# Kernel tuning notes

Measured on AMD Instinct MI355X. Metric: run time of the kernel, lower is better.

The kernel has to match this reference:

```python
import jax, jax.numpy as jnp
import numpy as np

DIMS = [3, 64, 64, 64, 3]  # [input_dim] + hidden dims + [input_dim]
TOTAL_W = sum(DIMS[l] * DIMS[l + 1] + 4 * DIMS[l + 1] for l in range(len(DIMS) - 1))  # 9356


def setup_inputs() -> dict:
    key = jax.random.key(0)
    k1, k2, k3 = jax.random.split(key, 3)
    B, N = 64, 8192
    context = jax.random.normal(k1, (B, N), dtype=jnp.float32)
    y = jax.random.normal(k2, (B, N, DIMS[0]), dtype=jnp.float32)
    tnw = jax.random.normal(k3, (B, TOTAL_W), dtype=jnp.float32) * 0.1
    return {"context": context, "y": y, "target_networks_weights": tnw}


def reference(context, y, target_networks_weights):
    B = target_networks_weights.shape[0]
    dx = y  # [B, N, dims[0]]
    i = 0
    n_layers = len(DIMS) - 1
    for l in range(n_layers):
        dl, dl1 = DIMS[l], DIMS[l + 1]
        W = target_networks_weights[:, i:i + dl * dl1].reshape(B, dl, dl1)
        i += dl * dl1
        bias = target_networks_weights[:, i:i + dl1]          # [B, dl1]
        i += dl1
        w_scale = target_networks_weights[:, i:i + dl1]        # [B, dl1]
        i += dl1
        b_scale = target_networks_weights[:, i:i + dl1]        # [B, dl1]
        i += dl1
        w_shift = target_networks_weights[:, i:i + dl1]        # [B, dl1]
        i += dl1
        # batched matmul + bias
        dx = jnp.einsum('bnd,bde->bne', dx, W) + bias[:, None, :]
        # sigmoid gate: bmm(context[:, :, None], w_scale[:, None, :]) = outer product
        scale = jax.nn.sigmoid(context[:, :, None] * w_scale[:, None, :] + b_scale[:, None, :])
        dx = scale * dx
        # shift term
        dx = dx + context[:, :, None] * w_shift[:, None, :]
        if l < n_layers - 1:
            dx = jax.nn.softplus(dx)
    return dx
```

## Files before the change

kernel.cpp:

```cpp
#include <hip/hip_runtime.h>
#include <math.h>

#define BB 64
#define NN 8192
#define TOTAL_W 9356

typedef _Float16 f16x8 __attribute__((ext_vector_type(8)));
typedef float f32x4 __attribute__((ext_vector_type(4)));
typedef unsigned int u32x2 __attribute__((ext_vector_type(2)));

#define L2E 1.44269504088896340736f
#define LN2 0.6931471805599453f

#define W0_OFF   0
#define FILM_OFF 1024
#define A1_OFF   (FILM_OFF + 4096)
#define A2_OFF   (A1_OFF + 8192)
#define A3_OFF   (A2_OFF + 8192)
#define ACT_OFF  (A3_OFF + 2048)
#define LDS_BYTES (ACT_OFF + 128*128)

#define MFMA16(a, b, c) __builtin_amdgcn_mfma_f32_16x16x32_f16(a, b, c, 0, 0, 0)

template<bool SP>
__device__ __forceinline__ void film_pack_store(unsigned char* smem, int Lf, int m, int g,
                                                float ctx, int pt, f32x4 acc) {
  float sp[4];
#pragma unroll
  for (int j = 0; j < 4; ++j) {
    f32x4 fm = *(const f32x4*)(smem + FILM_OFF + (((Lf * 64) + 16 * m + 4 * g + j) << 4));
    float pre = acc[j] + fm.w;
    float z = fmaf(ctx, fm.x, fm.y);
    float s = __builtin_amdgcn_rcpf(1.0f + __builtin_amdgcn_exp2f(-z));
    float v = fmaf(ctx, fm.z, s * pre);
    if (SP) {
      float u = __builtin_amdgcn_exp2f(v * L2E);
      v = LN2 * __builtin_amdgcn_logf(1.0f + u);
    }
    sp[j] = v;
  }
  auto p01 = __builtin_amdgcn_cvt_pkrtz(sp[0], sp[1]);
  auto p23 = __builtin_amdgcn_cvt_pkrtz(sp[2], sp[3]);
  u32x2 w;
  w.x = __builtin_bit_cast(unsigned int, p01);
  w.y = __builtin_bit_cast(unsigned int, p23);
  int slot = 4 * m + g;
  *(u32x2*)(smem + ACT_OFF + pt * 128 + (((slot ^ (pt & 14))) << 3)) = w;
}

__global__ __launch_bounds__(256)
void ode_hypernet_kernel(const float* __restrict__ context,
                         const float* __restrict__ y,
                         const float* __restrict__ tnw,
                         float* __restrict__ out) {
  __shared__ __align__(16) unsigned char smem[LDS_BYTES];
  const int b = blockIdx.y;
  const int tid = threadIdx.x;
  const float* __restrict__ wb = tnw + (size_t)b * TOTAL_W;

  if (tid < 64) {
    f32x4 v = {wb[tid], wb[64 + tid], wb[128 + tid], 0.f};
    *(f32x4*)(smem + W0_OFF + (tid << 4)) = v;
  }
  {
    const int biaso[4] = {192, 4544, 8896, 9344};
    const int dim[4] = {64, 64, 64, 3};
#pragma unroll
    for (int l = 0; l < 4; ++l) {
      if (tid < 64) {
        f32x4 v = {0.f, 0.f, 0.f, 0.f};
        if (tid < dim[l]) {
          int bo = biaso[l], d = dim[l];
          v.x = wb[bo + d + tid] * L2E;
          v.y = wb[bo + 2 * d + tid] * L2E;
          v.z = wb[bo + 3 * d + tid];
          v.w = wb[bo + tid];
        }
        *(f32x4*)(smem + FILM_OFF + ((l * 64 + tid) << 4)) = v;
      }
    }
  }
#pragma unroll
  for (int L = 0; L < 2; ++L) {
    const int woff = L ? 4800 : 448;
    const int aoff = L ? A2_OFF : A1_OFF;
    for (int r = tid; r < 512; r += 256) {
      int lane_r = r & 63;
      int t = (r >> 6) & 1;
      int m = r >> 7;
      int f_out = 16 * m + (lane_r & 15);
      int f_in0 = 32 * t + 8 * (lane_r >> 4);
      f16x8 h;
#pragma unroll
      for (int i = 0; i < 8; ++i) h[i] = (_Float16)wb[woff + (f_in0 + i) * 64 + f_out];
      *(f16x8*)(smem + aoff + r * 16) = h;
    }
  }
  if (tid < 128) {
    int lane_r = tid & 63;
    int t = tid >> 6;
    int f_out = lane_r & 15;
    int f_in0 = 32 * t + 8 * (lane_r >> 4);
    f16x8 h;
#pragma unroll
    for (int i = 0; i < 8; ++i)
      h[i] = (f_out < 3) ? (_Float16)wb[9152 + (f_in0 + i) * 3 + f_out] : (_Float16)0.f;
    *(f16x8*)(smem + A3_OFF + tid * 16) = h;
  }
  __syncthreads();

  const int lane = tid & 63;
  const int wid = tid >> 6;
  const int g = lane >> 4;
  const int col = lane & 15;
  const int pt0 = wid * 32 + col;
  const int pt1 = pt0 + 16;
  const int n0 = blockIdx.x * 128 + pt0;
  const int n1 = n0 + 16;

  const float ctx0 = context[(size_t)b * NN + n0];
  const float ctx1 = context[(size_t)b * NN + n1];
  const size_t yb0 = ((size_t)b * NN + n0) * 3;
  const size_t yb1 = ((size_t)b * NN + n1) * 3;
  const float y00 = y[yb0], y01 = y[yb0 + 1], y02 = y[yb0 + 2];
  const float y10 = y[yb1], y11 = y[yb1 + 1], y12 = y[yb1 + 2];

#pragma unroll
  for (int m = 0; m < 4; ++m) {
    f32x4 c0, c1;
#pragma unroll
    for (int j = 0; j < 4; ++j) {
      f32x4 w0 = *(const f32x4*)(smem + W0_OFF + ((16 * m + 4 * g + j) << 4));
      c0[j] = fmaf(y00, w0.x, fmaf(y01, w0.y, y02 * w0.z));
      c1[j] = fmaf(y10, w0.x, fmaf(y11, w0.y, y12 * w0.z));
    }
    film_pack_store<true>(smem, 0, m, g, ctx0, pt0, c0);
    film_pack_store<true>(smem, 0, m, g, ctx1, pt1, c1);
  }

  const int msk0 = pt0 & 14, msk1 = pt1 & 14;

#pragma unroll
  for (int L = 1; L <= 2; ++L) {
    const int aoff = (L == 1) ? A1_OFF : A2_OFF;
    f16x8 B00 = *(const f16x8*)(smem + ACT_OFF + pt0 * 128 + (((2 * g) ^ msk0) << 3));
    f16x8 B01 = *(const f16x8*)(smem + ACT_OFF + pt0 * 128 + (((8 + 2 * g) ^ msk0) << 3));
    f16x8 B10 = *(const f16x8*)(smem + ACT_OFF + pt1 * 128 + (((2 * g) ^ msk1) << 3));
    f16x8 B11 = *(const f16x8*)(smem + ACT_OFF + pt1 * 128 + (((8 + 2 * g) ^ msk1) << 3));
#pragma unroll
    for (int m = 0; m < 4; ++m) {
      f16x8 a0 = *(const f16x8*)(smem + aoff + ((m * 2 + 0) * 64 + lane) * 16);
      f16x8 a1 = *(const f16x8*)(smem + aoff + ((m * 2 + 1) * 64 + lane) * 16);
      f32x4 c0 = {0.f, 0.f, 0.f, 0.f};
      c0 = MFMA16(a0, B00, c0);
      c0 = MFMA16(a1, B01, c0);
      f32x4 c1 = {0.f, 0.f, 0.f, 0.f};
      c1 = MFMA16(a0, B10, c1);
      c1 = MFMA16(a1, B11, c1);
      film_pack_store<true>(smem, L, m, g, ctx0, pt0, c0);
      film_pack_store<true>(smem, L, m, g, ctx1, pt1, c1);
    }
  }

  {
    f16x8 B00 = *(const f16x8*)(smem + ACT_OFF + pt0 * 128 + (((2 * g) ^ msk0) << 3));
    f16x8 B01 = *(const f16x8*)(smem + ACT_OFF + pt0 * 128 + (((8 + 2 * g) ^ msk0) << 3));
    f16x8 B10 = *(const f16x8*)(smem + ACT_OFF + pt1 * 128 + (((2 * g) ^ msk1) << 3));
    f16x8 B11 = *(const f16x8*)(smem + ACT_OFF + pt1 * 128 + (((8 + 2 * g) ^ msk1) << 3));
    f16x8 a0 = *(const f16x8*)(smem + A3_OFF + (0 * 64 + lane) * 16);
    f16x8 a1 = *(const f16x8*)(smem + A3_OFF + (1 * 64 + lane) * 16);
    f32x4 c0 = {0.f, 0.f, 0.f, 0.f};
    c0 = MFMA16(a0, B00, c0);
    c0 = MFMA16(a1, B01, c0);
    f32x4 c1 = {0.f, 0.f, 0.f, 0.f};
    c1 = MFMA16(a0, B10, c1);
    c1 = MFMA16(a1, B11, c1);
#pragma unroll
    for (int p = 0; p < 2; ++p) {
      f32x4 c = p ? c1 : c0;
      float ctx = p ? ctx1 : ctx0;
      int n = p ? n1 : n0;
#pragma unroll
      for (int j = 0; j < 3; ++j) {
        f32x4 fm = *(const f32x4*)(smem + FILM_OFF + ((3 * 64 + 4 * g + j) << 4));
        float pre = c[j] + fm.w;
        float z = fmaf(ctx, fm.x, fm.y);
        float s = __builtin_amdgcn_rcpf(1.0f + __builtin_amdgcn_exp2f(-z));
        float v = fmaf(ctx, fm.z, s * pre);
        if (g == 0) out[((size_t)b * NN + n) * 3 + j] = v;
      }
    }
  }
}

extern "C" void kernel_launch(void* const* d_in, const int* in_sizes, int n_in,
                              void* d_out, int out_size, void* d_ws, size_t ws_size,
                              hipStream_t stream) {
  const float* context = (const float*)d_in[0];
  const float* y       = (const float*)d_in[1];
  const float* tnw     = (const float*)d_in[2];
  float* out           = (float*)d_out;

  dim3 grid(NN / 128, BB, 1);
  dim3 block(256, 1, 1);
  ode_hypernet_kernel<<<grid, block, 0, stream>>>(context, y, tnw, out);
}
```

Measured before the change: 61.33 us.

## Process two point tiles per block, SoA FiLM params, packed FMA epilogue

Each block now handles 256 points in two sequential halves, which halves the grid and amortizes the per-batch weight staging (fp16 conversion of the 64x64 matrices and FiLM parameters) over twice as many points. FiLM parameters are stored struct-of-arrays so that one vector LDS load fetches four outputs' worth of each parameter. Biases are folded into the MFMA accumulator init, the FiLM/softplus epilogue uses packed 2-wide FMAs, and the activation swizzle is changed to 16-byte granularity. The cost is fewer blocks for occupancy and latency hiding, plus a serialized loop over the two halves.

```diff
diff --git a/kernel.cpp b/kernel.cpp
--- a/kernel.cpp
+++ b/kernel.cpp
@@ -7,6 +7,7 @@
 
 typedef _Float16 f16x8 __attribute__((ext_vector_type(8)));
 typedef float f32x4 __attribute__((ext_vector_type(4)));
+typedef float f32x2 __attribute__((ext_vector_type(2)));
 typedef unsigned int u32x2 __attribute__((ext_vector_type(2)));
 
 #define L2E 1.44269504088896340736f
@@ -21,31 +22,56 @@
 #define LDS_BYTES (ACT_OFF + 128*128)
 
 #define MFMA16(a, b, c) __builtin_amdgcn_mfma_f32_16x16x32_f16(a, b, c, 0, 0, 0)
+#define EXP2 __builtin_amdgcn_exp2f
+#define LOG2 __builtin_amdgcn_logf
+#define RCPF __builtin_amdgcn_rcpf
+
+__device__ __forceinline__ f32x2 pfma(f32x2 a, f32x2 b, f32x2 c) {
+  return __builtin_elementwise_fma(a, b, c);
+}
+
+__device__ __forceinline__ f32x4 filmq(const unsigned char* smem, int l, int prm, int q) {
+  return *(const f32x4*)(smem + FILM_OFF + (((l * 4 + prm) * 64 + q) << 2));
+}
 
 template<bool SP>
-__device__ __forceinline__ void film_pack_store(unsigned char* smem, int Lf, int m, int g,
-                                                float ctx, int pt, f32x4 acc) {
-  float sp[4];
-#pragma unroll
-  for (int j = 0; j < 4; ++j) {
-    f32x4 fm = *(const f32x4*)(smem + FILM_OFF + (((Lf * 64) + 16 * m + 4 * g + j) << 4));
-    float pre = acc[j] + fm.w;
-    float z = fmaf(ctx, fm.x, fm.y);
-    float s = __builtin_amdgcn_rcpf(1.0f + __builtin_amdgcn_exp2f(-z));
-    float v = fmaf(ctx, fm.z, s * pre);
-    if (SP) {
-      float u = __builtin_amdgcn_exp2f(v * L2E);
-      v = LN2 * __builtin_amdgcn_logf(1.0f + u);
-    }
-    sp[j] = v;
-  }
-  auto p01 = __builtin_amdgcn_cvt_pkrtz(sp[0], sp[1]);
-  auto p23 = __builtin_amdgcn_cvt_pkrtz(sp[2], sp[3]);
+__device__ __forceinline__ u32x2 film_quad(f32x4 acc, float ctx,
+                                           f32x4 wscq, f32x4 bscq, f32x4 wshq) {
+  f32x2 ctx2 = {ctx, ctx};
+  f32x2 one = {1.f, 1.f};
+  f32x2 z0 = pfma(ctx2, (f32x2){wscq.x, wscq.y}, (f32x2){bscq.x, bscq.y});
+  f32x2 z1 = pfma(ctx2, (f32x2){wscq.z, wscq.w}, (f32x2){bscq.z, bscq.w});
+  f32x2 d0 = {EXP2(-z0.x), EXP2(-z0.y)};  d0 += one;
+  f32x2 d1 = {EXP2(-z1.x), EXP2(-z1.y)};  d1 += one;
+  f32x2 s0 = {RCPF(d0.x), RCPF(d0.y)};
+  f32x2 s1 = {RCPF(d1.x), RCPF(d1.y)};
+  f32x2 v0 = pfma(ctx2, (f32x2){wshq.x, wshq.y}, s0 * (f32x2){acc.x, acc.y});
+  f32x2 v1 = pfma(ctx2, (f32x2){wshq.z, wshq.w}, s1 * (f32x2){acc.z, acc.w});
+  if (SP) {
+    f32x2 l2 = {L2E, L2E}, ln = {LN2, LN2};
+    f32x2 t0 = v0 * l2, t1 = v1 * l2;
+    f32x2 u0 = {EXP2(t0.x), EXP2(t0.y)};  u0 += one;
+    f32x2 u1 = {EXP2(t1.x), EXP2(t1.y)};  u1 += one;
+    f32x2 g0 = {LOG2(u0.x), LOG2(u0.y)};
+    f32x2 g1 = {LOG2(u1.x), LOG2(u1.y)};
+    v0 = g0 * ln;
+    v1 = g1 * ln;
+  }
+  auto p01 = __builtin_amdgcn_cvt_pkrtz(v0.x, v0.y);
+  auto p23 = __builtin_amdgcn_cvt_pkrtz(v1.x, v1.y);
   u32x2 w;
   w.x = __builtin_bit_cast(unsigned int, p01);
   w.y = __builtin_bit_cast(unsigned int, p23);
-  int slot = 4 * m + g;
-  *(u32x2*)(smem + ACT_OFF + pt * 128 + (((slot ^ (pt & 14))) << 3)) = w;
+  return w;
+}
+
+__device__ __forceinline__ void act_store(unsigned char* smem, int pt, int slot, u32x2 w) {
+  int pos = ((((slot >> 1) ^ (pt & 7)) << 1) | (slot & 1));
+  *(u32x2*)(smem + ACT_OFF + pt * 128 + (pos << 3)) = w;
+}
+__device__ __forceinline__ f16x8 act_load(const unsigned char* smem, int pt, int pair) {
+  int gr = pair ^ (pt & 7);
+  return *(const f16x8*)(smem + ACT_OFF + pt * 128 + (gr << 4));
 }
 
 __global__ __launch_bounds__(256)
@@ -58,26 +84,25 @@
   const int tid = threadIdx.x;
   const float* __restrict__ wb = tnw + (size_t)b * TOTAL_W;
 
+  if (tid < 192) ((float*)(smem + W0_OFF))[tid] = wb[tid];
   if (tid < 64) {
-    f32x4 v = {wb[tid], wb[64 + tid], wb[128 + tid], 0.f};
-    *(f32x4*)(smem + W0_OFF + (tid << 4)) = v;
-  }
-  {
     const int biaso[4] = {192, 4544, 8896, 9344};
     const int dim[4] = {64, 64, 64, 3};
 #pragma unroll
     for (int l = 0; l < 4; ++l) {
-      if (tid < 64) {
-        f32x4 v = {0.f, 0.f, 0.f, 0.f};
-        if (tid < dim[l]) {
-          int bo = biaso[l], d = dim[l];
-          v.x = wb[bo + d + tid] * L2E;
-          v.y = wb[bo + 2 * d + tid] * L2E;
-          v.z = wb[bo + 3 * d + tid];
-          v.w = wb[bo + tid];
-        }
-        *(f32x4*)(smem + FILM_OFF + ((l * 64 + tid) << 4)) = v;
+      float bv = 0.f, wscv = 0.f, bscv = 0.f, wshv = 0.f;
+      if (tid < dim[l]) {
+        int bo = biaso[l], d = dim[l];
+        bv = wb[bo + tid];
+        wscv = wb[bo + d + tid] * L2E;
+        bscv = wb[bo + 2 * d + tid] * L2E;
+        wshv = wb[bo + 3 * d + tid];
       }
+      float* f = (float*)(smem + FILM_OFF) + l * 256;
+      f[tid] = bv;
+      f[64 + tid] = wscv;
+      f[128 + tid] = bscv;
+      f[192 + tid] = wshv;
     }
   }
 #pragma unroll
@@ -115,79 +140,104 @@
   const int col = lane & 15;
   const int pt0 = wid * 32 + col;
   const int pt1 = pt0 + 16;
-  const int n0 = blockIdx.x * 128 + pt0;
-  const int n1 = n0 + 16;
-
-  const float ctx0 = context[(size_t)b * NN + n0];
-  const float ctx1 = context[(size_t)b * NN + n1];
-  const size_t yb0 = ((size_t)b * NN + n0) * 3;
-  const size_t yb1 = ((size_t)b * NN + n1) * 3;
-  const float y00 = y[yb0], y01 = y[yb0 + 1], y02 = y[yb0 + 2];
-  const float y10 = y[yb1], y11 = y[yb1 + 1], y12 = y[yb1 + 2];
-
-#pragma unroll
-  for (int m = 0; m < 4; ++m) {
-    f32x4 c0, c1;
-#pragma unroll
-    for (int j = 0; j < 4; ++j) {
-      f32x4 w0 = *(const f32x4*)(smem + W0_OFF + ((16 * m + 4 * g + j) << 4));
-      c0[j] = fmaf(y00, w0.x, fmaf(y01, w0.y, y02 * w0.z));
-      c1[j] = fmaf(y10, w0.x, fmaf(y11, w0.y, y12 * w0.z));
-    }
-    film_pack_store<true>(smem, 0, m, g, ctx0, pt0, c0);
-    film_pack_store<true>(smem, 0, m, g, ctx1, pt1, c1);
-  }
-
-  const int msk0 = pt0 & 14, msk1 = pt1 & 14;
-
-#pragma unroll
-  for (int L = 1; L <= 2; ++L) {
-    const int aoff = (L == 1) ? A1_OFF : A2_OFF;
-    f16x8 B00 = *(const f16x8*)(smem + ACT_OFF + pt0 * 128 + (((2 * g) ^ msk0) << 3));
-    f16x8 B01 = *(const f16x8*)(smem + ACT_OFF + pt0 * 128 + (((8 + 2 * g) ^ msk0) << 3));
-    f16x8 B10 = *(const f16x8*)(smem + ACT_OFF + pt1 * 128 + (((2 * g) ^ msk1) << 3));
-    f16x8 B11 = *(const f16x8*)(smem + ACT_OFF + pt1 * 128 + (((8 + 2 * g) ^ msk1) << 3));
+  const int q4 = 4 * g;
+
+#pragma unroll 1
+  for (int half = 0; half < 2; ++half) {
+    const int nbase = blockIdx.x * 256 + half * 128;
+    const int n0 = nbase + pt0, n1 = nbase + pt1;
+    const float ctx0 = context[(size_t)b * NN + n0];
+    const float ctx1 = context[(size_t)b * NN + n1];
+    const size_t yb0 = ((size_t)b * NN + n0) * 3;
+    const size_t yb1 = ((size_t)b * NN + n1) * 3;
+    const float y00 = y[yb0], y01 = y[yb0 + 1], y02 = y[yb0 + 2];
+    const float y10 = y[yb1], y11 = y[yb1 + 1], y12 = y[yb1 + 2];
+
 #pragma unroll
     for (int m = 0; m < 4; ++m) {
-      f16x8 a0 = *(const f16x8*)(smem + aoff + ((m * 2 + 0) * 64 + lane) * 16);
-      f16x8 a1 = *(const f16x8*)(smem + aoff + ((m * 2 + 1) * 64 + lane) * 16);
-      f32x4 c0 = {0.f, 0.f, 0.f, 0.f};
+      const int q = 16 * m + q4;
+      f32x4 biasq = filmq(smem, 0, 0, q);
+      f32x4 w0a = *(const f32x4*)(smem + W0_OFF + ((0 * 64 + q) << 2));
+      f32x4 w0b = *(const f32x4*)(smem + W0_OFF + ((1 * 64 + q) << 2));
+      f32x4 w0c = *(const f32x4*)(smem + W0_OFF + ((2 * 64 + q) << 2));
+      f32x2 aLo, aHi, cLo, cHi;
+      aLo = pfma((f32x2){y00, y00}, (f32x2){w0a.x, w0a.y}, (f32x2){biasq.x, biasq.y});
+      aLo = pfma((f32x2){y01, y01}, (f32x2){w0b.x, w0b.y}, aLo);
+      aLo = pfma((f32x2){y02, y02}, (f32x2){w0c.x, w0c.y}, aLo);
+      aHi = pfma((f32x2){y00, y00}, (f32x2){w0a.z, w0a.w}, (f32x2){biasq.z, biasq.w});
+      aHi = pfma((f32x2){y01, y01}, (f32x2){w0b.z, w0b.w}, aHi);
+      aHi = pfma((f32x2){y02, y02}, (f32x2){w0c.z, w0c.w}, aHi);
+      cLo = pfma((f32x2){y10, y10}, (f32x2){w0a.x, w0a.y}, (f32x2){biasq.x, biasq.y});
+      cLo = pfma((f32x2){y11, y11}, (f32x2){w0b.x, w0b.y}, cLo);
+      cLo = pfma((f32x2){y12, y12}, (f32x2){w0c.x, w0c.y}, cLo);
+      cHi = pfma((f32x2){y10, y10}, (f32x2){w0a.z, w0a.w}, (f32x2){biasq.z, biasq.w});
+      cHi = pfma((f32x2){y11, y11}, (f32x2){w0b.z, w0b.w}, cHi);
+      cHi = pfma((f32x2){y12, y12}, (f32x2){w0c.z, w0c.w}, cHi);
+      f32x4 acc0 = {aLo.x, aLo.y, aHi.x, aHi.y};
+      f32x4 acc1 = {cLo.x, cLo.y, cHi.x, cHi.y};
+      f32x4 wscq = filmq(smem, 0, 1, q);
+      f32x4 bscq = filmq(smem, 0, 2, q);
+      f32x4 wshq = filmq(smem, 0, 3, q);
+      act_store(smem, pt0, 4 * m + g, film_quad<true>(acc0, ctx0, wscq, bscq, wshq));
+      act_store(smem, pt1, 4 * m + g, film_quad<true>(acc1, ctx1, wscq, bscq, wshq));
+    }
+
+#pragma unroll
+    for (int L = 1; L <= 2; ++L) {
+      const int aoff = (L == 1) ? A1_OFF : A2_OFF;
+      f16x8 B00 = act_load(smem, pt0, g);
+      f16x8 B01 = act_load(smem, pt0, 4 + g);
+      f16x8 B10 = act_load(smem, pt1, g);
+      f16x8 B11 = act_load(smem, pt1, 4 + g);
+#pragma unroll
+      for (int m = 0; m < 4; ++m) {
+        const int q = 16 * m + q4;
+        f32x4 biasq = filmq(smem, L, 0, q);
+        f16x8 a0 = *(const f16x8*)(smem + aoff + ((m * 2 + 0) * 64 + lane) * 16);
+        f16x8 a1 = *(const f16x8*)(smem + aoff + ((m * 2 + 1) * 64 + lane) * 16);
+        f32x4 c0 = biasq, c1 = biasq;
+        c0 = MFMA16(a0, B00, c0);
+        c0 = MFMA16(a1, B01, c0);
+        c1 = MFMA16(a0, B10, c1);
+        c1 = MFMA16(a1, B11, c1);
+        f32x4 wscq = filmq(smem, L, 1, q);
+        f32x4 bscq = filmq(smem, L, 2, q);
+        f32x4 wshq = filmq(smem, L, 3, q);
+        act_store(smem, pt0, 4 * m + g, film_quad<true>(c0, ctx0, wscq, bscq, wshq));
+        act_store(smem, pt1, 4 * m + g, film_quad<true>(c1, ctx1, wscq, bscq, wshq));
+      }
+    }
+
+    {
+      f16x8 B00 = act_load(smem, pt0, g);
+      f16x8 B01 = act_load(smem, pt0, 4 + g);
+      f16x8 B10 = act_load(smem, pt1, g);
+      f16x8 B11 = act_load(smem, pt1, 4 + g);
+      f16x8 a0 = *(const f16x8*)(smem + A3_OFF + (0 * 64 + lane) * 16);
+      f16x8 a1 = *(const f16x8*)(smem + A3_OFF + (1 * 64 + lane) * 16);
+      f32x4 biasq = filmq(smem, 3, 0, q4);
+      f32x4 c0 = biasq, c1 = biasq;
       c0 = MFMA16(a0, B00, c0);
       c0 = MFMA16(a1, B01, c0);
-      f32x4 c1 = {0.f, 0.f, 0.f, 0.f};
       c1 = MFMA16(a0, B10, c1);
       c1 = MFMA16(a1, B11, c1);
-      film_pack_store<true>(smem, L, m, g, ctx0, pt0, c0);
-      film_pack_store<true>(smem, L, m, g, ctx1, pt1, c1);
-    }
-  }
-
-  {
-    f16x8 B00 = *(const f16x8*)(smem + ACT_OFF + pt0 * 128 + (((2 * g) ^ msk0) << 3));
-    f16x8 B01 = *(const f16x8*)(smem + ACT_OFF + pt0 * 128 + (((8 + 2 * g) ^ msk0) << 3));
-    f16x8 B10 = *(const f16x8*)(smem + ACT_OFF + pt1 * 128 + (((2 * g) ^ msk1) << 3));
-    f16x8 B11 = *(const f16x8*)(smem + ACT_OFF + pt1 * 128 + (((8 + 2 * g) ^ msk1) << 3));
-    f16x8 a0 = *(const f16x8*)(smem + A3_OFF + (0 * 64 + lane) * 16);
-    f16x8 a1 = *(const f16x8*)(smem + A3_OFF + (1 * 64 + lane) * 16);
-    f32x4 c0 = {0.f, 0.f, 0.f, 0.f};
-    c0 = MFMA16(a0, B00, c0);
-    c0 = MFMA16(a1, B01, c0);
-    f32x4 c1 = {0.f, 0.f, 0.f, 0.f};
-    c1 = MFMA16(a0, B10, c1);
-    c1 = MFMA16(a1, B11, c1);
-#pragma unroll
-    for (int p = 0; p < 2; ++p) {
-      f32x4 c = p ? c1 : c0;
-      float ctx = p ? ctx1 : ctx0;
-      int n = p ? n1 : n0;
-#pragma unroll
-      for (int j = 0; j < 3; ++j) {
-        f32x4 fm = *(const f32x4*)(smem + FILM_OFF + ((3 * 64 + 4 * g + j) << 4));
-        float pre = c[j] + fm.w;
-        float z = fmaf(ctx, fm.x, fm.y);
-        float s = __builtin_amdgcn_rcpf(1.0f + __builtin_amdgcn_exp2f(-z));
-        float v = fmaf(ctx, fm.z, s * pre);
-        if (g == 0) out[((size_t)b * NN + n) * 3 + j] = v;
+      f32x4 wscq = filmq(smem, 3, 1, q4);
+      f32x4 bscq = filmq(smem, 3, 2, q4);
+      f32x4 wshq = filmq(smem, 3, 3, q4);
+      if (g == 0) {
+#pragma unroll
+        for (int p = 0; p < 2; ++p) {
+          f32x4 c = p ? c1 : c0;
+          float ctx = p ? ctx1 : ctx0;
+          int n = p ? n1 : n0;
+#pragma unroll
+          for (int j = 0; j < 3; ++j) {
+            float z = fmaf(ctx, wscq[j], bscq[j]);
+            float s = RCPF(1.0f + EXP2(-z));
+            float v = fmaf(ctx, wshq[j], s * c[j]);
+            out[((size_t)b * NN + n) * 3 + j] = v;
+          }
+        }
       }
     }
   }
@@ -201,7 +251,7 @@
   const float* tnw     = (const float*)d_in[2];
   float* out           = (float*)d_out;
 
-  dim3 grid(NN / 128, BB, 1);
+  dim3 grid(NN / 256, BB, 1);
   dim3 block(256, 1, 1);
   ode_hypernet_kernel<<<grid, block, 0, stream>>>(context, y, tnw, out);
 }
```

After: 53.56 us. 12.7% less time.
